# Optimization experiments

Hardware: AMD Instinct MI355X
Metric: run time of the kernel (lower is better)

Reference implementation:

```python
import jax, jax.numpy as jnp
import numpy as np

B, T, H, U = 32, 2048, 512, 32

def _glorot(key, shape):
    fan_in, fan_out = shape[0], shape[1]
    limit = np.sqrt(6.0 / (fan_in + fan_out))
    return jax.random.uniform(key, shape, jnp.float32, -limit, limit)

def setup_inputs() -> dict:
    key = jax.random.key(0)
    ks = jax.random.split(key, 6)
    return {
        "x": jax.random.normal(ks[0], (B, T, H), jnp.float32),
        "t": jax.random.normal(ks[1], (B, T, H), jnp.float32),
        "kernel_x": _glorot(ks[2], (H, U)),
        "kernel_t": _glorot(ks[3], (H, U)),
        "kernel_a": _glorot(ks[4], (U, H)),
        "bias_x": jnp.zeros((U,), jnp.float32),
        "bias_t": jnp.zeros((U,), jnp.float32),
        "lambd": _glorot(ks[5], (T, 1)),
    }

def reference(x, t, kernel_x, kernel_t, kernel_a, bias_x, bias_t, lambd):
    # gamma, beta: [B, T, U]
    gamma = jnp.tanh(jnp.einsum('bth,hu->btu', x, kernel_x) + bias_x)
    beta = jnp.tanh(jnp.einsum('bth,hu->btu', t, kernel_t) + bias_t)
    # per-timespan convex combination; lambd [T,1] broadcasts over units
    delta = lambd * gamma + (1.0 - lambd) * beta
    # scores [B, T, H]; softmax over the timespan axis (-2)
    scores = jnp.einsum('btu,uh->bth', delta, kernel_a)
    alpha = jax.nn.softmax(scores, axis=-2)
    return alpha
```

## Files before the change

kernel.cpp:

```cpp
#include <hip/hip_runtime.h>
#include <cmath>

#define Hdim 512
#define Udim 32
#define Bdim 32
#define Tdim 2048
#define RM   64
#define KC   32
#define CH   128

typedef __attribute__((ext_vector_type(8))) short bf16x8;
typedef __attribute__((ext_vector_type(4))) float f32x4;

__device__ __forceinline__ unsigned short f2bf(float f) {
    unsigned int u = __float_as_uint(f);
    u += 0x7FFFu + ((u >> 16) & 1u);
    return (unsigned short)(u >> 16);
}
__device__ __forceinline__ float bf2f(unsigned short h) {
    return __uint_as_float(((unsigned int)h) << 16);
}

__global__ __launch_bounds__(256, 4) void k1_gemm_act(
    const float* __restrict__ x, const float* __restrict__ tin,
    const float* __restrict__ kx, const float* __restrict__ kt,
    const float* __restrict__ bx, const float* __restrict__ bt,
    const float* __restrict__ lambd, float* __restrict__ delta)
{
    __shared__ short axh[2048], axl[2048], ath[2048], atl[2048];
    __shared__ short wxh[1024], wxl[1024], wth[1024], wtl[1024];

    const int tid  = threadIdx.x;
    const int lane = tid & 63;
    const int wv   = tid >> 6;
    const int row0 = blockIdx.x * RM;

    const int srow = tid >> 3;
    const int sk4  = tid & 7;
    const int aw_j0    = (sk4 & 1) * 4;
    const int aw_klane = 16 * (sk4 >> 1);
    const int su  = tid & 31;
    const int skq = tid >> 5;
    const int ww_idx = (su >> 4) * 512 + ((su & 15) + 16 * (skq >> 1)) * 8 + (skq & 1) * 4;

    const float4* xg = (const float4*)x;
    const float4* tg = (const float4*)tin;

    float4 px[2], pt[2];
    float  pwx[4], pwt[4];

    f32x4 accx[2], acct_[2];
#pragma unroll
    for (int ut = 0; ut < 2; ++ut) {
        accx[ut]  = (f32x4){0.f, 0.f, 0.f, 0.f};
        acct_[ut] = (f32x4){0.f, 0.f, 0.f, 0.f};
    }

#pragma unroll
    for (int l = 0; l < 2; ++l) {
        const size_t row = (size_t)(row0 + srow + 32 * l);
        px[l] = xg[row * (Hdim / 4) + sk4];
        pt[l] = tg[row * (Hdim / 4) + sk4];
    }
#pragma unroll
    for (int i = 0; i < 4; ++i) {
        pwx[i] = kx[(size_t)(skq * 4 + i) * Udim + su];
        pwt[i] = kt[(size_t)(skq * 4 + i) * Udim + su];
    }

#pragma unroll 1
    for (int c = 0; c < Hdim / KC; ++c) {
        __syncthreads();

#pragma unroll
        for (int l = 0; l < 2; ++l) {
            const int r   = srow + 32 * l;
            const int idx = (r >> 4) * 512 + ((r & 15) + aw_klane) * 8 + aw_j0;
            float4 v = px[l];
            unsigned short h0 = f2bf(v.x), h1 = f2bf(v.y), h2 = f2bf(v.z), h3 = f2bf(v.w);
            *(short4*)&axh[idx] = make_short4((short)h0, (short)h1, (short)h2, (short)h3);
            *(short4*)&axl[idx] = make_short4(
                (short)f2bf(v.x - bf2f(h0)), (short)f2bf(v.y - bf2f(h1)),
                (short)f2bf(v.z - bf2f(h2)), (short)f2bf(v.w - bf2f(h3)));
            v = pt[l];
            h0 = f2bf(v.x); h1 = f2bf(v.y); h2 = f2bf(v.z); h3 = f2bf(v.w);
            *(short4*)&ath[idx] = make_short4((short)h0, (short)h1, (short)h2, (short)h3);
            *(short4*)&atl[idx] = make_short4(
                (short)f2bf(v.x - bf2f(h0)), (short)f2bf(v.y - bf2f(h1)),
                (short)f2bf(v.z - bf2f(h2)), (short)f2bf(v.w - bf2f(h3)));
        }
        {
            unsigned short h0 = f2bf(pwx[0]), h1 = f2bf(pwx[1]), h2 = f2bf(pwx[2]), h3 = f2bf(pwx[3]);
            *(short4*)&wxh[ww_idx] = make_short4((short)h0, (short)h1, (short)h2, (short)h3);
            *(short4*)&wxl[ww_idx] = make_short4(
                (short)f2bf(pwx[0] - bf2f(h0)), (short)f2bf(pwx[1] - bf2f(h1)),
                (short)f2bf(pwx[2] - bf2f(h2)), (short)f2bf(pwx[3] - bf2f(h3)));
            h0 = f2bf(pwt[0]); h1 = f2bf(pwt[1]); h2 = f2bf(pwt[2]); h3 = f2bf(pwt[3]);
            *(short4*)&wth[ww_idx] = make_short4((short)h0, (short)h1, (short)h2, (short)h3);
            *(short4*)&wtl[ww_idx] = make_short4(
                (short)f2bf(pwt[0] - bf2f(h0)), (short)f2bf(pwt[1] - bf2f(h1)),
                (short)f2bf(pwt[2] - bf2f(h2)), (short)f2bf(pwt[3] - bf2f(h3)));
        }

        if (c + 1 < Hdim / KC) {
            const int cn = c + 1;
#pragma unroll
            for (int l = 0; l < 2; ++l) {
                const size_t row = (size_t)(row0 + srow + 32 * l);
                px[l] = xg[row * (Hdim / 4) + cn * (KC / 4) + sk4];
                pt[l] = tg[row * (Hdim / 4) + cn * (KC / 4) + sk4];
            }
#pragma unroll
            for (int i = 0; i < 4; ++i) {
                pwx[i] = kx[(size_t)(cn * KC + skq * 4 + i) * Udim + su];
                pwt[i] = kt[(size_t)(cn * KC + skq * 4 + i) * Udim + su];
            }
        }

        __syncthreads();

        const int ab = wv * 512 + lane * 8;
        bf16x8 Axh = *(const bf16x8*)&axh[ab];
        bf16x8 Axl = *(const bf16x8*)&axl[ab];
        bf16x8 Ath = *(const bf16x8*)&ath[ab];
        bf16x8 Atl = *(const bf16x8*)&atl[ab];
#pragma unroll
        for (int ut = 0; ut < 2; ++ut) {
            const int wb = ut * 512 + lane * 8;
            bf16x8 Bh = *(const bf16x8*)&wxh[wb];
            bf16x8 Bl = *(const bf16x8*)&wxl[wb];
            accx[ut] = __builtin_amdgcn_mfma_f32_16x16x32_bf16(Axh, Bh, accx[ut], 0, 0, 0);
            accx[ut] = __builtin_amdgcn_mfma_f32_16x16x32_bf16(Axh, Bl, accx[ut], 0, 0, 0);
            accx[ut] = __builtin_amdgcn_mfma_f32_16x16x32_bf16(Axl, Bh, accx[ut], 0, 0, 0);
            Bh = *(const bf16x8*)&wth[wb];
            Bl = *(const bf16x8*)&wtl[wb];
            acct_[ut] = __builtin_amdgcn_mfma_f32_16x16x32_bf16(Ath, Bh, acct_[ut], 0, 0, 0);
            acct_[ut] = __builtin_amdgcn_mfma_f32_16x16x32_bf16(Ath, Bl, acct_[ut], 0, 0, 0);
            acct_[ut] = __builtin_amdgcn_mfma_f32_16x16x32_bf16(Atl, Bh, acct_[ut], 0, 0, 0);
        }
    }

    const int crow = (lane >> 4) * 4;
    const int ccol = lane & 15;
    const float bx0 = bx[ccol],      bt0 = bt[ccol];
    const float bx1 = bx[16 + ccol], bt1 = bt[16 + ccol];
#pragma unroll
    for (int r = 0; r < 4; ++r) {
        const int grow = row0 + wv * 16 + crow + r;
        const float lam = lambd[grow & (Tdim - 1)];
        float g0  = tanhf(accx[0][r] + bx0);
        float be0 = tanhf(acct_[0][r] + bt0);
        float g1  = tanhf(accx[1][r] + bx1);
        float be1 = tanhf(acct_[1][r] + bt1);
        delta[(size_t)grow * Udim + ccol]      = lam * g0 + (1.0f - lam) * be0;
        delta[(size_t)grow * Udim + 16 + ccol] = lam * g1 + (1.0f - lam) * be1;
    }
}

__global__ __launch_bounds__(1024, 2) void k2_softmax(
    const float* __restrict__ delta, const float* __restrict__ ka_g,
    float* __restrict__ alpha)
{
    __shared__ float dsm[2][CH * Udim];
    __shared__ float ms[16][64];
    __shared__ float ls[16][64];

    const int tid = threadIdx.x;
    const int tx  = tid & 63;
    const int ty  = tid >> 6;
    const int b   = blockIdx.x & 31;
    const int ht  = blockIdx.x >> 5;
    const int h   = ht * 64 + tx;

    float ka[Udim];
#pragma unroll
    for (int u = 0; u < Udim; ++u) ka[u] = ka_g[u * Hdim + h];

    const float4* dsrc = (const float4*)(delta + (size_t)b * Tdim * Udim);

    ((float4*)dsm[0])[tid] = dsrc[tid];

    float m = -1e30f, l = 0.f;
#pragma unroll 1
    for (int c = 0; c < Tdim / CH; ++c) {
        __syncthreads();
        const float* cur = dsm[c & 1];
        if (c + 1 < Tdim / CH)
            ((float4*)dsm[(c + 1) & 1])[tid] = dsrc[(size_t)(c + 1) * (CH * Udim / 4) + tid];
#pragma unroll
        for (int i = 0; i < CH / 16; ++i) {
            const int r = ty + 16 * i;
            const float4* dp = (const float4*)(cur + r * Udim);
            float4 q[8];
#pragma unroll
            for (int j = 0; j < 8; ++j) q[j] = dp[j];
            float s0 = 0.f, s1 = 0.f, s2 = 0.f, s3 = 0.f;
#pragma unroll
            for (int j = 0; j < 8; ++j) {
                s0 = fmaf(q[j].x, ka[4 * j],     s0);
                s1 = fmaf(q[j].y, ka[4 * j + 1], s1);
                s2 = fmaf(q[j].z, ka[4 * j + 2], s2);
                s3 = fmaf(q[j].w, ka[4 * j + 3], s3);
            }
            const float s = (s0 + s1) + (s2 + s3);
            const float mn = fmaxf(m, s);
            l = l * __expf(m - mn) + __expf(s - mn);
            m = mn;
        }
    }

    ms[ty][tx] = m;
    ls[ty][tx] = l;
    __syncthreads();
    float M = -1e30f;
#pragma unroll
    for (int w = 0; w < 16; ++w) M = fmaxf(M, ms[w][tx]);
    float L = 0.f;
#pragma unroll
    for (int w = 0; w < 16; ++w) L += ls[w][tx] * __expf(ms[w][tx] - M);
    const float rinv = 1.0f / L;

    ((float4*)dsm[0])[tid] = dsrc[tid];

    float* abase = alpha + (size_t)b * Tdim * Hdim + h;
#pragma unroll 1
    for (int c = 0; c < Tdim / CH; ++c) {
        __syncthreads();
        const float* cur = dsm[c & 1];
        if (c + 1 < Tdim / CH)
            ((float4*)dsm[(c + 1) & 1])[tid] = dsrc[(size_t)(c + 1) * (CH * Udim / 4) + tid];
#pragma unroll
        for (int i = 0; i < CH / 16; ++i) {
            const int r = ty + 16 * i;
            const int t = c * CH + r;
            const float4* dp = (const float4*)(cur + r * Udim);
            float4 q[8];
#pragma unroll
            for (int j = 0; j < 8; ++j) q[j] = dp[j];
            float s0 = 0.f, s1 = 0.f, s2 = 0.f, s3 = 0.f;
#pragma unroll
            for (int j = 0; j < 8; ++j) {
                s0 = fmaf(q[j].x, ka[4 * j],     s0);
                s1 = fmaf(q[j].y, ka[4 * j + 1], s1);
                s2 = fmaf(q[j].z, ka[4 * j + 2], s2);
                s3 = fmaf(q[j].w, ka[4 * j + 3], s3);
            }
            const float s = (s0 + s1) + (s2 + s3);
            abase[(size_t)t * Hdim] = __expf(s - M) * rinv;
        }
    }
}

extern "C" void kernel_launch(void* const* d_in, const int* in_sizes, int n_in,
                              void* d_out, int out_size, void* d_ws, size_t ws_size,
                              hipStream_t stream) {
    const float* x     = (const float*)d_in[0];
    const float* tin   = (const float*)d_in[1];
    const float* kx    = (const float*)d_in[2];
    const float* kt    = (const float*)d_in[3];
    const float* ka    = (const float*)d_in[4];
    const float* bx    = (const float*)d_in[5];
    const float* bt    = (const float*)d_in[6];
    const float* lambd = (const float*)d_in[7];
    float* alpha = (float*)d_out;
    float* delta = (float*)d_ws;

    k1_gemm_act<<<(Bdim * Tdim) / RM, 256, 0, stream>>>(x, tin, kx, kt, bx, bt, lambd, delta);
    k2_softmax<<<256, 1024, 0, stream>>>(delta, ka, alpha);
}
```

Measured before the change: 435.2 us.

## Drop LDS staging in softmax kernel, prefetch delta rows into registers

The softmax kernel no longer copies delta through double-buffered shared memory guarded by barriers. Each half-wave now covers 32 output columns for one timestep and loads delta rows straight from global memory (cache broadcast) into registers, prefetching the next row while computing the current one. Blocks shrink to 512 threads and the grid doubles to 512 blocks, and the online-softmax update becomes a branch that skips one exponential. The aim is to cut barrier and LDS overhead and raise occupancy, at the cost of narrower 128-byte store segments per half-wave and more global or L1 load traffic.

```diff
diff --git a/kernel.cpp b/kernel.cpp
--- a/kernel.cpp
+++ b/kernel.cpp
@@ -7,7 +7,6 @@
 #define Tdim 2048
 #define RM   64
 #define KC   32
-#define CH   128
 
 typedef __attribute__((ext_vector_type(8))) short bf16x8;
 typedef __attribute__((ext_vector_type(4))) float f32x4;
@@ -157,20 +156,20 @@
     }
 }
 
-__global__ __launch_bounds__(1024, 2) void k2_softmax(
+__global__ __launch_bounds__(512, 4) void k2_softmax(
     const float* __restrict__ delta, const float* __restrict__ ka_g,
     float* __restrict__ alpha)
 {
-    __shared__ float dsm[2][CH * Udim];
-    __shared__ float ms[16][64];
-    __shared__ float ls[16][64];
-
-    const int tid = threadIdx.x;
-    const int tx  = tid & 63;
-    const int ty  = tid >> 6;
-    const int b   = blockIdx.x & 31;
-    const int ht  = blockIdx.x >> 5;
-    const int h   = ht * 64 + tx;
+    __shared__ float ms[16][32];
+    __shared__ float ls[16][32];
+
+    const int tid  = threadIdx.x;
+    const int tx   = tid & 63;
+    const int hx   = tx & 31;
+    const int st   = (tid >> 6) * 2 + (tx >> 5);
+    const int b    = blockIdx.x & 31;
+    const int ht   = blockIdx.x >> 5;
+    const int h    = ht * 32 + hx;
 
     float ka[Udim];
 #pragma unroll
@@ -178,22 +177,21 @@
 
     const float4* dsrc = (const float4*)(delta + (size_t)b * Tdim * Udim);
 
-    ((float4*)dsm[0])[tid] = dsrc[tid];
-
     float m = -1e30f, l = 0.f;
-#pragma unroll 1
-    for (int c = 0; c < Tdim / CH; ++c) {
-        __syncthreads();
-        const float* cur = dsm[c & 1];
-        if (c + 1 < Tdim / CH)
-            ((float4*)dsm[(c + 1) & 1])[tid] = dsrc[(size_t)(c + 1) * (CH * Udim / 4) + tid];
-#pragma unroll
-        for (int i = 0; i < CH / 16; ++i) {
-            const int r = ty + 16 * i;
-            const float4* dp = (const float4*)(cur + r * Udim);
-            float4 q[8];
-#pragma unroll
-            for (int j = 0; j < 8; ++j) q[j] = dp[j];
+    {
+        float4 q[8], nq[8];
+        {
+            const float4* p = dsrc + (size_t)st * (Udim / 4);
+#pragma unroll
+            for (int j = 0; j < 8; ++j) q[j] = p[j];
+        }
+#pragma unroll 2
+        for (int i = 0; i < Tdim / 16; ++i) {
+            const int tn = st + 16 * ((i + 1) & (Tdim / 16 - 1));
+            const float4* np = dsrc + (size_t)tn * (Udim / 4);
+#pragma unroll
+            for (int j = 0; j < 8; ++j) nq[j] = np[j];
+
             float s0 = 0.f, s1 = 0.f, s2 = 0.f, s3 = 0.f;
 #pragma unroll
             for (int j = 0; j < 8; ++j) {
@@ -203,40 +201,39 @@
                 s3 = fmaf(q[j].w, ka[4 * j + 3], s3);
             }
             const float s = (s0 + s1) + (s2 + s3);
-            const float mn = fmaxf(m, s);
-            l = l * __expf(m - mn) + __expf(s - mn);
-            m = mn;
-        }
-    }
-
-    ms[ty][tx] = m;
-    ls[ty][tx] = l;
+            if (s > m) { l = l * __expf(m - s) + 1.0f; m = s; }
+            else       { l += __expf(s - m); }
+#pragma unroll
+            for (int j = 0; j < 8; ++j) q[j] = nq[j];
+        }
+    }
+
+    ms[st][hx] = m;
+    ls[st][hx] = l;
     __syncthreads();
     float M = -1e30f;
 #pragma unroll
-    for (int w = 0; w < 16; ++w) M = fmaxf(M, ms[w][tx]);
+    for (int w = 0; w < 16; ++w) M = fmaxf(M, ms[w][hx]);
     float L = 0.f;
 #pragma unroll
-    for (int w = 0; w < 16; ++w) L += ls[w][tx] * __expf(ms[w][tx] - M);
+    for (int w = 0; w < 16; ++w) L += ls[w][hx] * __expf(ms[w][hx] - M);
     const float rinv = 1.0f / L;
 
-    ((float4*)dsm[0])[tid] = dsrc[tid];
-
     float* abase = alpha + (size_t)b * Tdim * Hdim + h;
-#pragma unroll 1
-    for (int c = 0; c < Tdim / CH; ++c) {
-        __syncthreads();
-        const float* cur = dsm[c & 1];
-        if (c + 1 < Tdim / CH)
-            ((float4*)dsm[(c + 1) & 1])[tid] = dsrc[(size_t)(c + 1) * (CH * Udim / 4) + tid];
-#pragma unroll
-        for (int i = 0; i < CH / 16; ++i) {
-            const int r = ty + 16 * i;
-            const int t = c * CH + r;
-            const float4* dp = (const float4*)(cur + r * Udim);
-            float4 q[8];
-#pragma unroll
-            for (int j = 0; j < 8; ++j) q[j] = dp[j];
+    {
+        float4 q[8], nq[8];
+        {
+            const float4* p = dsrc + (size_t)st * (Udim / 4);
+#pragma unroll
+            for (int j = 0; j < 8; ++j) q[j] = p[j];
+        }
+#pragma unroll 2
+        for (int i = 0; i < Tdim / 16; ++i) {
+            const int tn = st + 16 * ((i + 1) & (Tdim / 16 - 1));
+            const float4* np = dsrc + (size_t)tn * (Udim / 4);
+#pragma unroll
+            for (int j = 0; j < 8; ++j) nq[j] = np[j];
+
             float s0 = 0.f, s1 = 0.f, s2 = 0.f, s3 = 0.f;
 #pragma unroll
             for (int j = 0; j < 8; ++j) {
@@ -246,7 +243,10 @@
                 s3 = fmaf(q[j].w, ka[4 * j + 3], s3);
             }
             const float s = (s0 + s1) + (s2 + s3);
+            const int t = st + 16 * i;
             abase[(size_t)t * Hdim] = __expf(s - M) * rinv;
+#pragma unroll
+            for (int j = 0; j < 8; ++j) q[j] = nq[j];
         }
     }
 }
@@ -266,5 +266,5 @@
     float* delta = (float*)d_ws;
 
     k1_gemm_act<<<(Bdim * Tdim) / RM, 256, 0, stream>>>(x, tin, kx, kt, bx, bt, lambd, delta);
-    k2_softmax<<<256, 1024, 0, stream>>>(delta, ka, alpha);
-}
+    k2_softmax<<<512, 512, 0, stream>>>(delta, ka, alpha);
+}
```

New measurement: 555.5 us. 1.28x slower.
